# Optimization experiments

Measured on AMD Instinct MI355X. Metric: run time of the kernel, lower is better.

The kernel has to match this reference:

```python
import jax, jax.numpy as jnp
from jax import lax
import numpy as np

DN = ('NHWC', 'HWIO', 'NHWC')


def extract_patches(x, k, stride):
    # tf.image.extract_patches with sizes [1,k,k,1], strides [1,s,s,1], SAME padding.
    # Output depth ordering matches TF: (ki, kj, channel).
    B, H, W, C = x.shape
    oh = -(-H // stride)
    ow = -(-W // stride)
    ph = max((oh - 1) * stride + k - H, 0)
    pw = max((ow - 1) * stride + k - W, 0)
    xp = jnp.pad(x, ((0, 0), (ph // 2, ph - ph // 2), (pw // 2, pw - pw // 2), (0, 0)))
    cols = [xp[:, i:i + stride * (oh - 1) + 1:stride, j:j + stride * (ow - 1) + 1:stride, :]
            for i in range(k) for j in range(k)]
    return jnp.stack(cols, axis=3).reshape(B, oh, ow, k * k * C)


def contextual_attention(x, mask_s, rate=2, fuse_k=3, softmax_scale=10.0):
    B, H, W, C = x.shape
    k = rate * 2 - 1  # 3
    # raw (full-resolution) patches used as deconv filters: [B,k,k,C,L]
    raw = extract_patches(x, k, rate)
    h, w = raw.shape[1], raw.shape[2]
    L = h * w
    raw_f = raw.reshape(B, L, k, k, C).transpose(0, 2, 3, 4, 1)
    # downsample src/ref by rate (extract_patches with size 1 == strided slice)
    src = x[:, ::rate, ::rate, :]  # [B,h,w,C]
    feats = extract_patches(src, k, 1).reshape(B, L, k, k, C).transpose(0, 2, 3, 4, 1)  # [B,k,k,C,L]
    # NOTE: source normalizes by sum of squares over axes (0,1,2) = (batch,kh,kw) -> [C,L], no sqrt
    denom = jnp.maximum(jnp.sum(feats * feats, axis=(0, 1, 2)), 1e-8)
    ref_feat = feats / denom
    # mask: maxpool 16/16 then 3/1, then invert
    m = lax.reduce_window(mask_s, -jnp.inf, lax.max, (1, 16, 16, 1), (1, 16, 16, 1), 'SAME')
    m = lax.reduce_window(m, -jnp.inf, lax.max, (1, 3, 3, 1), (1, 1, 1, 1), 'SAME')
    mm = 1.0 - m  # [B,h,w,1]
    # per-sample correlation: conv src_b with its own normalized patch bank
    corr = lambda s, f: lax.conv_general_dilated(s[None], f, (1, 1), 'SAME', dimension_numbers=DN)[0]
    y = jax.vmap(corr)(src, ref_feat)  # [B,h,w,L]
    # fuse: diagonal (identity) 3x3 convs over the (query, key) score plane, both orderings
    fuse_w = jnp.eye(fuse_k, dtype=x.dtype).reshape(fuse_k, fuse_k, 1, 1)
    yi = y.reshape(B, h * w, L, 1)
    yi = lax.conv_general_dilated(yi, fuse_w, (1, 1), 'SAME', dimension_numbers=DN)
    yi = yi.reshape(B, h, w, h, w).transpose(0, 2, 1, 4, 3).reshape(B, h * w, L, 1)
    yi = lax.conv_general_dilated(yi, fuse_w, (1, 1), 'SAME', dimension_numbers=DN)
    y = yi.reshape(B, w, h, w, h).transpose(0, 2, 1, 4, 3).reshape(B, h, w, L)
    # masked softmax over reference patches
    y = jax.nn.softmax(y * mm * softmax_scale, axis=-1) * mm
    # per-sample transposed conv (paste raw patches), matching tf.nn.conv2d_transpose SAME stride=rate
    pt = max((h - 1) * rate + k - H, 0)
    pl = max((w - 1) * rate + k - W, 0)
    pad_h = (k - 1 - pt // 2, k - 1 - (pt - pt // 2))
    pad_w = (k - 1 - pl // 2, k - 1 - (pl - pl // 2))

    def deconv(y_b, f_b):
        wg = jnp.flip(f_b, axis=(0, 1)).swapaxes(2, 3)  # [k,k,L,C]
        return lax.conv_general_dilated(y_b[None], wg, (1, 1), (pad_h, pad_w),
                                        lhs_dilation=(rate, rate), dimension_numbers=DN)[0]

    y_up = jax.vmap(deconv)(y, raw_f)  # [B,H,W,C]
    return y_up, y


def gated_conv(x, w, b, dw, pw, db):
    # gen_conv_gated_ds: Conv2D -> ELU gated by SeparableConv2D -> channel softmax
    x1 = jax.nn.elu(lax.conv_general_dilated(x, w, (1, 1), 'SAME', dimension_numbers=DN) + b)
    x2 = lax.conv_general_dilated(x, dw, (1, 1), 'SAME', feature_group_count=x.shape[-1],
                                  dimension_numbers=DN)
    x2 = lax.conv_general_dilated(x2, pw, (1, 1), 'SAME', dimension_numbers=DN) + db
    return x1 * jax.nn.softmax(x2, axis=-1)


def setup_inputs():
    key = jax.random.key(0)
    ks = jax.random.split(key, 8)
    B, H, W, C, dim = 8, 64, 64, 128, 128
    s = 0.05
    x = jax.random.normal(ks[0], (B, H, W, C), jnp.float32)
    mask_s = jnp.zeros((B, 16 * H // 2, 16 * W // 2, 1), jnp.float32)
    mask_s = mask_s.at[:, 128:384, 128:384, :].set(1.0)
    return {
        'x': x,
        'mask_s': mask_s,
        'w1': jax.random.normal(ks[1], (3, 3, C, dim), jnp.float32) * s,
        'b1': jnp.zeros((dim,), jnp.float32),
        'dw1': jax.random.normal(ks[2], (3, 3, 1, C), jnp.float32) * s,
        'pw1': jax.random.normal(ks[3], (1, 1, C, dim), jnp.float32) * s,
        'db1': jnp.zeros((dim,), jnp.float32),
        'w2': jax.random.normal(ks[4], (3, 3, dim + C, dim), jnp.float32) * s,
        'b2': jnp.zeros((dim,), jnp.float32),
        'dw2': jax.random.normal(ks[5], (3, 3, 1, dim + C), jnp.float32) * s,
        'pw2': jax.random.normal(ks[6], (1, 1, dim + C, dim), jnp.float32) * s,
        'db2': jnp.zeros((dim,), jnp.float32),
    }


def reference(x, mask_s, w1, b1, dw1, pw1, db1, w2, b2, dw2, pw2, db2):
    y_up, corres = contextual_attention(x, mask_s)
    a = gated_conv(y_up, w1, b1, dw1, pw1, db1)
    a = jnp.concatenate([a, x], axis=3)
    a = gated_conv(a, w2, b2, dw2, pw2, db2)
    return a, corres
```

## Files before the change

kernel.cpp:

```cpp
#include <hip/hip_runtime.h>
#include <hip/hip_bf16.h>


#define BOFF_SP      0
#define BOFF_INVD    4734976
#define BOFF_SP16    5259264
#define BOFF_BF16    7626752
#define BOFF_T       0
#define BOFF_BP16    0
#define BOFF_YP16    33554432
#define BOFF_YUP     50331648
#define BOFF_SM      0
#define BOFF_P316    16777216
#define BOFF_A1      25698304
#define BOFF_X16     42475520
#define BOFF_WT1     69238784
#define BOFF_WT2     69828608
#define BOFF_PW1     71008256
#define BOFF_PW2     71041024
#define BOFF_M0      71106560
#define BOFF_MM      71139328

typedef float f32x4 __attribute__((ext_vector_type(4)));
typedef _Float16 f16x8 __attribute__((ext_vector_type(8)));

__global__ __launch_bounds__(256) void k_mask_pool(const float* __restrict__ mask, float* __restrict__ m0) {
    int blk = blockIdx.x;
    int b = blk >> 10, pq = blk & 1023, p = pq >> 5, q = pq & 31;
    int t = threadIdx.x, dy = t >> 4, dx = t & 15;
    float v = mask[((size_t)(b * 512 + p * 16 + dy)) * 512 + q * 16 + dx];
#pragma unroll
    for (int o = 32; o; o >>= 1) v = fmaxf(v, __shfl_xor(v, o));
    __shared__ float s[4];
    if ((t & 63) == 0) s[t >> 6] = v;
    __syncthreads();
    if (t == 0) m0[blk] = fmaxf(fmaxf(s[0], s[1]), fmaxf(s[2], s[3]));
}

__global__ void k_mask_dilate(const float* __restrict__ m0, float* __restrict__ mm) {
    int idx = blockIdx.x * 256 + threadIdx.x;
    if (idx >= 8192) return;
    int b = idx >> 10, pq = idx & 1023, p = pq >> 5, q = pq & 31;
    float v = -1e30f;
    for (int di = -1; di <= 1; ++di)
        for (int dj = -1; dj <= 1; ++dj) {
            int pp = p + di, qq = q + dj;
            if (pp >= 0 && pp < 32 && qq >= 0 && qq < 32)
                v = fmaxf(v, m0[(b << 10) + pp * 32 + qq]);
        }
    mm[idx] = 1.0f - v;
}

__global__ void k_srcpad(const float* __restrict__ x, float* __restrict__ sp,
                         _Float16* __restrict__ sp16) {
    int idx = blockIdx.x * 256 + threadIdx.x;
    if (idx >= 8 * 34 * 34 * 128) return;
    int c = idx & 127;
    int r = idx >> 7;
    int xx = r % 34; r /= 34;
    int yy = r % 34; int b = r / 34;
    float v = 0.f;
    if (yy >= 1 && yy <= 32 && xx >= 1 && xx <= 32)
        v = x[(((size_t)(b * 64 + (yy - 1) * 2)) * 64 + (xx - 1) * 2) * 128 + c];
    sp[idx] = v;
    sp16[idx] = (_Float16)v;
}

__global__ void k_invd(const float* __restrict__ sp, float* __restrict__ invd) {
    int idx = blockIdx.x * 256 + threadIdx.x;
    if (idx >= 1024 * 128) return;
    int c = idx & 127, l = idx >> 7, lh = l >> 5, lw = l & 31;
    float s = 0.f;
    for (int b = 0; b < 8; ++b)
#pragma unroll
        for (int i = 0; i < 3; ++i)
#pragma unroll
            for (int j = 0; j < 3; ++j) {
                float v = sp[(((size_t)(b * 34 + lh + i)) * 34 + (lw + j)) * 128 + c];
                s += v * v;
            }
    invd[idx] = 1.0f / fmaxf(s, 1e-8f);
}

__global__ void k_corr_B16(const float* __restrict__ sp, const float* __restrict__ invd,
                           _Float16* __restrict__ bf) {
    int idx = blockIdx.x * 256 + threadIdx.x;
    if (idx >= 1179648) return;
    int c8 = idx & 15; int rest = idx >> 4;
    int ij = rest % 9; int rest2 = rest / 9;
    int l = rest2 & 1023, b = rest2 >> 10;
    int lh = l >> 5, lw = l & 31;
    int i = (ij >= 6) ? 2 : (ij >= 3 ? 1 : 0);
    int j = ij - 3 * i;
    int c0 = c8 * 8;
    const float* s = sp + (((size_t)(b * 34 + lh + i)) * 34 + (lw + j)) * 128 + c0;
    const float* dv = invd + l * 128 + c0;
    f16x8 h;
#pragma unroll
    for (int u = 0; u < 8; ++u) h[u] = (_Float16)(s[u] * dv[u]);
    size_t off = ((size_t)(b * 1024 + l)) * 1152 + ij * 128 + c0;
    *reinterpret_cast<f16x8*>(bf + off) = h;
}

__global__ void k_deconv_B16(const float* __restrict__ x, _Float16* __restrict__ bp) {
    int idx = blockIdx.x * 256 + threadIdx.x;
    if (idx >= 1179648) return;
    int l8 = idx & 127; int rest = idx >> 7;
    int c = rest & 127; int rest2 = rest >> 7;
    int ij = rest2 % 9; int b = rest2 / 9;
    int ip = (ij >= 6) ? 2 : (ij >= 3 ? 1 : 0);
    int jp = ij - 3 * ip;
    int l0 = l8 * 8;
    int lh = l0 >> 5, lw0 = l0 & 31;
    int rr = 2 * lh + ip;
    f16x8 h;
#pragma unroll
    for (int u = 0; u < 8; ++u) {
        int ss = 2 * (lw0 + u) + jp;
        float v = (rr < 64 && ss < 64) ? x[(((size_t)(b * 64 + rr)) * 64 + ss) * 128 + c] : 0.f;
        h[u] = (_Float16)v;
    }
    size_t off = (((size_t)(b * 9 + ij)) * 128 + c) * 1024 + l0;
    *reinterpret_cast<f16x8*>(bp + off) = h;
}

__global__ __launch_bounds__(256) void k_corr_mfma(const _Float16* __restrict__ sp16,
                                                   const _Float16* __restrict__ bf,
                                                   float* __restrict__ outy) {
    const int bid = blockIdx.x;
    const int xcd = bid & 7, slot = bid >> 3;
    const int tm = slot & 15, pg = slot >> 4;
    const int panel = pg * 8 + xcd;
    const int b = panel >> 3, tn = panel & 7;
    __shared__ _Float16 Aa[64][40];
    __shared__ _Float16 Ab[64][40];
    const int tid = threadIdx.x;
    const int w = tid >> 6, lane = tid & 63, m = lane & 15, g = lane >> 4;
    f32x4 acc[4][2];
#pragma unroll
    for (int mf = 0; mf < 4; ++mf)
#pragma unroll
        for (int nn = 0; nn < 2; ++nn) acc[mf][nn] = f32x4{0.f, 0.f, 0.f, 0.f};
    const int srow = tid >> 2, scc = (tid & 3) * 8;
    const int pq = tm * 64 + srow, p = pq >> 5, q = pq & 31;
    const int col0 = tn * 128 + w * 32 + m;
    const size_t boff0 = ((size_t)b * 1024 + col0) * 1152 + g * 8;
    const size_t boff1 = ((size_t)b * 1024 + col0 + 16) * 1152 + g * 8;

    auto aoff = [&](int kt) -> size_t {
        int ij = kt >> 7;
        int i = (ij >= 6) ? 2 : (ij >= 3 ? 1 : 0);
        int j = ij - 3 * i;
        int c0 = (kt & 127) + scc;
        return (((size_t)(b * 34 + p + i)) * 34 + (q + j)) * 128 + c0;
    };
    f16x8 aq_a = *reinterpret_cast<const f16x8*>(sp16 + aoff(0));
    f16x8 aq_b = *reinterpret_cast<const f16x8*>(sp16 + aoff(32));
    f16x8 aq2_a = *reinterpret_cast<const f16x8*>(sp16 + aoff(64));
    f16x8 aq2_b = *reinterpret_cast<const f16x8*>(sp16 + aoff(96));
    f16x8 b0q_a = *reinterpret_cast<const f16x8*>(bf + boff0);
    f16x8 b0q_b = *reinterpret_cast<const f16x8*>(bf + boff0 + 32);
    f16x8 b1q_a = *reinterpret_cast<const f16x8*>(bf + boff1);
    f16x8 b1q_b = *reinterpret_cast<const f16x8*>(bf + boff1 + 32);
    f16x8 b0q2_a = *reinterpret_cast<const f16x8*>(bf + boff0 + 64);
    f16x8 b0q2_b = *reinterpret_cast<const f16x8*>(bf + boff0 + 96);
    f16x8 b1q2_a = *reinterpret_cast<const f16x8*>(bf + boff1 + 64);
    f16x8 b1q2_b = *reinterpret_cast<const f16x8*>(bf + boff1 + 96);

    for (int kt = 0; kt < 1152; kt += 64) {
        __syncthreads();
        *reinterpret_cast<f16x8*>(&Aa[srow][scc]) = aq_a;
        *reinterpret_cast<f16x8*>(&Ab[srow][scc]) = aq_b;
        __syncthreads();
        const int kt2 = (kt + 128 < 1152) ? kt + 128 : kt;
        f16x8 cb0a = b0q_a, cb0b = b0q_b, cb1a = b1q_a, cb1b = b1q_b;
        aq_a = aq2_a; aq_b = aq2_b;
        aq2_a = *reinterpret_cast<const f16x8*>(sp16 + aoff(kt2));
        aq2_b = *reinterpret_cast<const f16x8*>(sp16 + aoff(kt2 + 32));
        b0q_a = b0q2_a; b0q_b = b0q2_b;
        b1q_a = b1q2_a; b1q_b = b1q2_b;
        b0q2_a = *reinterpret_cast<const f16x8*>(bf + boff0 + kt2);
        b0q2_b = *reinterpret_cast<const f16x8*>(bf + boff0 + kt2 + 32);
        b1q2_a = *reinterpret_cast<const f16x8*>(bf + boff1 + kt2);
        b1q2_b = *reinterpret_cast<const f16x8*>(bf + boff1 + kt2 + 32);

        f16x8 av;
#pragma unroll
        for (int mf = 0; mf < 4; ++mf) {
            av = *reinterpret_cast<const f16x8*>(&Aa[mf * 16 + m][g * 8]);
            acc[mf][0] = __builtin_amdgcn_mfma_f32_16x16x32_f16(av, cb0a, acc[mf][0], 0, 0, 0);
            acc[mf][1] = __builtin_amdgcn_mfma_f32_16x16x32_f16(av, cb1a, acc[mf][1], 0, 0, 0);
            av = *reinterpret_cast<const f16x8*>(&Ab[mf * 16 + m][g * 8]);
            acc[mf][0] = __builtin_amdgcn_mfma_f32_16x16x32_f16(av, cb0b, acc[mf][0], 0, 0, 0);
            acc[mf][1] = __builtin_amdgcn_mfma_f32_16x16x32_f16(av, cb1b, acc[mf][1], 0, 0, 0);
        }
    }
#pragma unroll
    for (int mf = 0; mf < 4; ++mf) {
        int row = tm * 64 + mf * 16 + g * 4;
#pragma unroll
        for (int nn = 0; nn < 2; ++nn) {
            int col = col0 + nn * 16;
#pragma unroll
            for (int r = 0; r < 4; ++r)
                outy[((size_t)b << 20) + (size_t)(row + r) * 1024 + col] = acc[mf][nn][r];
        }
    }
}

__global__ __launch_bounds__(256) void k_deconv_mfma(const _Float16* __restrict__ yp16,
                                                     const _Float16* __restrict__ bp,
                                                     float* __restrict__ yup) {
    const int bid = blockIdx.x;
    const int b = bid & 7;
    const int slot = bid >> 3;
    const int tn = slot % 9;
    const int tm = slot / 9;
    __shared__ _Float16 Aa[64][40];
    __shared__ _Float16 Ab[64][40];
    const int tid = threadIdx.x;
    const int w = tid >> 6, lane = tid & 63, m = lane & 15, g = lane >> 4;
    f32x4 acc[4][2];
#pragma unroll
    for (int mf = 0; mf < 4; ++mf)
#pragma unroll
        for (int nn = 0; nn < 2; ++nn) acc[mf][nn] = f32x4{0.f, 0.f, 0.f, 0.f};
    const int srow = tid >> 2, scc = (tid & 3) * 8;
    const int c0 = w * 32 + m;
    const _Float16* abase = yp16 + ((size_t)b << 20) + (size_t)(tm * 64 + srow) * 1024 + scc;
    const size_t boff0 = (((size_t)(b * 9 + tn)) * 128 + c0) * 1024 + g * 8;
    const size_t boff1 = (((size_t)(b * 9 + tn)) * 128 + c0 + 16) * 1024 + g * 8;

    f16x8 aq_a = *reinterpret_cast<const f16x8*>(abase);
    f16x8 aq_b = *reinterpret_cast<const f16x8*>(abase + 32);
    f16x8 aq2_a = *reinterpret_cast<const f16x8*>(abase + 64);
    f16x8 aq2_b = *reinterpret_cast<const f16x8*>(abase + 96);
    f16x8 b0q_a = *reinterpret_cast<const f16x8*>(bp + boff0);
    f16x8 b0q_b = *reinterpret_cast<const f16x8*>(bp + boff0 + 32);
    f16x8 b1q_a = *reinterpret_cast<const f16x8*>(bp + boff1);
    f16x8 b1q_b = *reinterpret_cast<const f16x8*>(bp + boff1 + 32);
    f16x8 b0q2_a = *reinterpret_cast<const f16x8*>(bp + boff0 + 64);
    f16x8 b0q2_b = *reinterpret_cast<const f16x8*>(bp + boff0 + 96);
    f16x8 b1q2_a = *reinterpret_cast<const f16x8*>(bp + boff1 + 64);
    f16x8 b1q2_b = *reinterpret_cast<const f16x8*>(bp + boff1 + 96);

    for (int kt = 0; kt < 1024; kt += 64) {
        __syncthreads();
        *reinterpret_cast<f16x8*>(&Aa[srow][scc]) = aq_a;
        *reinterpret_cast<f16x8*>(&Ab[srow][scc]) = aq_b;
        __syncthreads();
        const int kt2 = (kt + 128 < 1024) ? kt + 128 : kt;
        f16x8 cb0a = b0q_a, cb0b = b0q_b, cb1a = b1q_a, cb1b = b1q_b;
        aq_a = aq2_a; aq_b = aq2_b;
        aq2_a = *reinterpret_cast<const f16x8*>(abase + kt2);
        aq2_b = *reinterpret_cast<const f16x8*>(abase + kt2 + 32);
        b0q_a = b0q2_a; b0q_b = b0q2_b;
        b1q_a = b1q2_a; b1q_b = b1q2_b;
        b0q2_a = *reinterpret_cast<const f16x8*>(bp + boff0 + kt2);
        b0q2_b = *reinterpret_cast<const f16x8*>(bp + boff0 + kt2 + 32);
        b1q2_a = *reinterpret_cast<const f16x8*>(bp + boff1 + kt2);
        b1q2_b = *reinterpret_cast<const f16x8*>(bp + boff1 + kt2 + 32);

        f16x8 av;
#pragma unroll
        for (int mf = 0; mf < 4; ++mf) {
            av = *reinterpret_cast<const f16x8*>(&Aa[mf * 16 + m][g * 8]);
            acc[mf][0] = __builtin_amdgcn_mfma_f32_16x16x32_f16(av, cb0a, acc[mf][0], 0, 0, 0);
            acc[mf][1] = __builtin_amdgcn_mfma_f32_16x16x32_f16(av, cb1a, acc[mf][1], 0, 0, 0);
            av = *reinterpret_cast<const f16x8*>(&Ab[mf * 16 + m][g * 8]);
            acc[mf][0] = __builtin_amdgcn_mfma_f32_16x16x32_f16(av, cb0b, acc[mf][0], 0, 0, 0);
            acc[mf][1] = __builtin_amdgcn_mfma_f32_16x16x32_f16(av, cb1b, acc[mf][1], 0, 0, 0);
        }
    }
    const int ip = (tn >= 6) ? 2 : (tn >= 3 ? 1 : 0);
    const int jp = tn - 3 * ip;
#pragma unroll
    for (int mf = 0; mf < 4; ++mf) {
        int uvb = tm * 64 + mf * 16 + g * 4;
#pragma unroll
        for (int nn = 0; nn < 2; ++nn) {
            int c = c0 + nn * 16;
#pragma unroll
            for (int r = 0; r < 4; ++r) {
                int uv = uvb + r;
                int uu = uv >> 5, vv = uv & 31;
                int P = 2 * uu + ip, Q = 2 * vv + jp;
                if (P < 64 && Q < 64)
                    atomicAdd(&yup[(((size_t)(b * 64 + P)) * 64 + Q) * 128 + c], acc[mf][nn][r]);
            }
        }
    }
}

__global__ void k_fuse12(const float* __restrict__ y, float* __restrict__ out) {
    size_t idx = (size_t)blockIdx.x * 256 + threadIdx.x;
    if (idx >= (size_t)8 * 1024 * 1024) return;
    int t = (int)(idx & 1023);
    int s = (int)((idx >> 10) & 1023);
    int b = (int)(idx >> 20);
    int m0 = ((s & 31) << 5) + (s >> 5);
    int n0 = ((t & 31) << 5) + (t >> 5);
    const float* base = y + ((size_t)b << 20);
    float v = 0.f;
#pragma unroll
    for (int d = -1; d <= 1; ++d) {
        int mm_ = m0 + d, nn_ = n0 + d;
        if (mm_ >= 0 && mm_ < 1024 && nn_ >= 0 && nn_ < 1024) {
            int a = ((mm_ & 31) << 5) + (mm_ >> 5);
            int c = ((nn_ & 31) << 5) + (nn_ >> 5);
            float zv = base[(size_t)a * 1024 + c];
            if (a > 0 && c > 0) zv += base[(size_t)(a - 1) * 1024 + (c - 1)];
            if (a < 1023 && c < 1023) zv += base[(size_t)(a + 1) * 1024 + (c + 1)];
            v += zv;
        }
    }
    out[idx] = v;
}

__global__ __launch_bounds__(256) void k_softmax1024(const float* __restrict__ yv,
                                                     const float* __restrict__ mm,
                                                     float* __restrict__ outc,
                                                     _Float16* __restrict__ yp16) {
    int row = blockIdx.x;
    const float* base = yv + (size_t)row * 1024;
    float mmv = mm[row];
    int t = threadIdx.x;
    float vals[4];
    float mx = -1e30f;
#pragma unroll
    for (int i = 0; i < 4; ++i) {
        vals[i] = base[t + i * 256] * mmv * 10.0f;
        mx = fmaxf(mx, vals[i]);
    }
#pragma unroll
    for (int o = 32; o; o >>= 1) mx = fmaxf(mx, __shfl_xor(mx, o));
    __shared__ float red[8];
    if ((t & 63) == 0) red[t >> 6] = mx;
    __syncthreads();
    mx = fmaxf(fmaxf(red[0], red[1]), fmaxf(red[2], red[3]));
    float s = 0.f;
#pragma unroll
    for (int i = 0; i < 4; ++i) {
        vals[i] = expf(vals[i] - mx);
        s += vals[i];
    }
#pragma unroll
    for (int o = 32; o; o >>= 1) s += __shfl_xor(s, o);
    if ((t & 63) == 0) red[4 + (t >> 6)] = s;
    __syncthreads();
    s = red[4] + red[5] + red[6] + red[7];
    float inv = mmv / s;
#pragma unroll
    for (int i = 0; i < 4; ++i) {
        float pv = vals[i] * inv;
        outc[(size_t)row * 1024 + t + i * 256] = pv;
        yp16[(size_t)row * 1024 + t + i * 256] = (_Float16)pv;
    }
}

__global__ __launch_bounds__(256) void k_pad16(const float* __restrict__ in,
                                               _Float16* __restrict__ o) {
    int idx = blockIdx.x * 256 + threadIdx.x;
    int c8 = idx & 15;
    int r = idx >> 4;
    int pc = r % 66; r /= 66;
    int pr = r % 66; int b = r / 66;
    f16x8 h;
    if (pr >= 1 && pr <= 64 && pc >= 1 && pc <= 64) {
        const float* s = in + (((size_t)(b * 64 + pr - 1)) * 64 + (pc - 1)) * 128 + c8 * 8;
        float4 v0 = *reinterpret_cast<const float4*>(s);
        float4 v1 = *reinterpret_cast<const float4*>(s + 4);
        h[0] = (_Float16)v0.x; h[1] = (_Float16)v0.y; h[2] = (_Float16)v0.z; h[3] = (_Float16)v0.w;
        h[4] = (_Float16)v1.x; h[5] = (_Float16)v1.y; h[6] = (_Float16)v1.z; h[7] = (_Float16)v1.w;
    } else {
#pragma unroll
        for (int u = 0; u < 8; ++u) h[u] = (_Float16)0.f;
    }
    *reinterpret_cast<f16x8*>(o + (size_t)idx * 8) = h;
}

__global__ void k_wt16(const float* __restrict__ w, _Float16* __restrict__ o, int CI) {
    int idx = blockIdx.x * 256 + threadIdx.x;
    if (idx >= 9 * CI * 128) return;
    int ci = idx % CI; int rest = idx / CI;
    int co = rest & 127; int ij = rest >> 7;
    o[idx] = (_Float16)w[((size_t)ij * CI + ci) * 128 + co];
}

__global__ void k_pw16(const float* __restrict__ pw, _Float16* __restrict__ out, int CI) {
    int idx = blockIdx.x * 256 + threadIdx.x;
    if (idx >= CI * 128) return;
    int co = idx & 127, ci = idx >> 7;
    out[(size_t)co * CI + ci] = (_Float16)pw[idx];
}

template <int CI>
__global__ __launch_bounds__(256) void k_dwpw_mfma(const _Float16* __restrict__ in0,
                                                   const _Float16* __restrict__ in1,
                                                   const float* __restrict__ dwW,
                                                   const _Float16* __restrict__ pwt,
                                                   const float* __restrict__ db,
                                                   float* __restrict__ smout) {
    const int bid = blockIdx.x;
    const int swz = (bid & 7) * 128 + (bid >> 3);
    const int b = swz >> 7;
    const int rem = swz & 127;
    const int P = rem >> 1, half = rem & 1;
    const int Q0 = half * 32;
    const int t = threadIdx.x;
    const int w = t >> 6, lane = t & 63, m = lane & 15, g = lane >> 4;
    __shared__ _Float16 Adw[32 * CI];
    __shared__ float red[2][4][32];
    char* ab = (char*)Adw;
    const int px = t & 31;
    const int grp = t >> 5;
    const int cb = grp * (CI / 8);
    float dwacc[CI / 8];
#pragma unroll
    for (int u = 0; u < CI / 8; ++u) dwacc[u] = 0.f;
#pragma unroll
    for (int i = 0; i < 3; ++i) {
#pragma unroll
        for (int j = 0; j < 3; ++j) {
            const int ij = i * 3 + j;
#pragma unroll
            for (int c8 = 0; c8 < CI / 64; ++c8) {
                const int c = cb + c8 * 8;
                const _Float16* ph = (CI == 256 && c >= 128) ? in1 : in0;
                const int cc = (CI == 256 && c >= 128) ? (c - 128) : c;
                size_t off = (((size_t)b * 66 + P + i) * 66 + Q0 + px + j) * 128 + cc;
                f16x8 vh = *reinterpret_cast<const f16x8*>(ph + off);
#pragma unroll
                for (int u = 0; u < 8; ++u)
                    dwacc[c8 * 8 + u] = fmaf((float)vh[u], dwW[ij * CI + c + u], dwacc[c8 * 8 + u]);
            }
        }
    }
#pragma unroll
    for (int c8 = 0; c8 < CI / 64; ++c8) {
        f16x8 hv;
#pragma unroll
        for (int u = 0; u < 8; ++u) hv[u] = (_Float16)dwacc[c8 * 8 + u];
        int byte = px * (CI * 2) + (cb + c8 * 8) * 2;
        int sz = byte ^ ((px & 7) << 4);
        *reinterpret_cast<f16x8*>(ab + sz) = hv;
    }
    __syncthreads();
    f32x4 acc[2][2];
#pragma unroll
    for (int mt = 0; mt < 2; ++mt)
#pragma unroll
        for (int nn = 0; nn < 2; ++nn) acc[mt][nn] = f32x4{0.f, 0.f, 0.f, 0.f};
    const int co0 = w * 32 + m;
#pragma unroll
    for (int kc = 0; kc < CI / 32; ++kc) {
        f16x8 av[2];
#pragma unroll
        for (int mt = 0; mt < 2; ++mt) {
            int prow = mt * 16 + m;
            int byte = prow * (CI * 2) + (kc * 32 + g * 8) * 2;
            int sz = byte ^ ((prow & 7) << 4);
            av[mt] = *reinterpret_cast<const f16x8*>(ab + sz);
        }
#pragma unroll
        for (int nn = 0; nn < 2; ++nn) {
            f16x8 bv = *reinterpret_cast<const f16x8*>(pwt + (size_t)(co0 + nn * 16) * CI + kc * 32 + g * 8);
#pragma unroll
            for (int mt = 0; mt < 2; ++mt)
                acc[mt][nn] = __builtin_amdgcn_mfma_f32_16x16x32_f16(av[mt], bv, acc[mt][nn], 0, 0, 0);
        }
    }
    float db0 = db[co0], db1 = db[co0 + 16];
    float mx[2][4];
#pragma unroll
    for (int mt = 0; mt < 2; ++mt)
#pragma unroll
        for (int r = 0; r < 4; ++r) {
            acc[mt][0][r] += db0;
            acc[mt][1][r] += db1;
            float v = fmaxf(acc[mt][0][r], acc[mt][1][r]);
#pragma unroll
            for (int o = 1; o <= 8; o <<= 1) v = fmaxf(v, __shfl_xor(v, o));
            mx[mt][r] = v;
        }
    if (m == 0) {
#pragma unroll
        for (int mt = 0; mt < 2; ++mt)
#pragma unroll
            for (int r = 0; r < 4; ++r) red[0][w][mt * 16 + g * 4 + r] = mx[mt][r];
    }
    __syncthreads();
    float sume[2][4];
#pragma unroll
    for (int mt = 0; mt < 2; ++mt)
#pragma unroll
        for (int r = 0; r < 4; ++r) {
            int p = mt * 16 + g * 4 + r;
            float M = fmaxf(fmaxf(red[0][0][p], red[0][1][p]), fmaxf(red[0][2][p], red[0][3][p]));
            acc[mt][0][r] = expf(acc[mt][0][r] - M);
            acc[mt][1][r] = expf(acc[mt][1][r] - M);
            float s = acc[mt][0][r] + acc[mt][1][r];
#pragma unroll
            for (int o = 1; o <= 8; o <<= 1) s += __shfl_xor(s, o);
            sume[mt][r] = s;
        }
    if (m == 0) {
#pragma unroll
        for (int mt = 0; mt < 2; ++mt)
#pragma unroll
            for (int r = 0; r < 4; ++r) red[1][w][mt * 16 + g * 4 + r] = sume[mt][r];
    }
    __syncthreads();
#pragma unroll
    for (int mt = 0; mt < 2; ++mt)
#pragma unroll
        for (int r = 0; r < 4; ++r) {
            int p = mt * 16 + g * 4 + r;
            float S = red[1][0][p] + red[1][1][p] + red[1][2][p] + red[1][3][p];
            float inv = 1.0f / S;
            size_t pix = ((size_t)b * 64 + P) * 64 + Q0 + p;
            smout[pix * 128 + co0] = acc[mt][0][r] * inv;
            smout[pix * 128 + co0 + 16] = acc[mt][1][r] * inv;
        }
}

template <int CI>
__global__ __launch_bounds__(256, 4) void k_conv_lds(const _Float16* __restrict__ in0,
                                                     const _Float16* __restrict__ in1,
                                                     const _Float16* __restrict__ wt,
                                                     const float* __restrict__ bias,
                                                     const float* __restrict__ sm,
                                                     float* __restrict__ out) {
    const int bid = blockIdx.x;
    const int idx = (bid & 7) * 128 + (bid >> 3);
    const int row = idx >> 1, cohalf = idx & 1;
    const int b = row >> 6, P = row & 63;
    const int tid = threadIdx.x;
    const int w = tid >> 6, lane = tid & 63;
    const int m = lane & 15, g = lane >> 4;
    __shared__ _Float16 S[66 * 128];
    char* sb = (char*)S;
    f32x4 acc[4];
#pragma unroll
    for (int mt = 0; mt < 4; ++mt) acc[mt] = f32x4{0.f, 0.f, 0.f, 0.f};
    const int cow = cohalf * 64 + w * 16 + m;

#pragma unroll
    for (int half = 0; half < CI / 128; ++half) {
        const _Float16* ih = (half == 0) ? in0 : in1;
        const size_t rbase0 = ((size_t)b * 66 + P) * 66 * 128;
#pragma unroll
        for (int i = 0; i < 3; ++i) {
            __syncthreads();
            const size_t rsrc = rbase0 + (size_t)i * 66 * 128;
#pragma unroll
            for (int e0 = 0; e0 < 1056; e0 += 256) {
                int e = e0 + tid;
                if (e < 1056) {
                    int px = e >> 4, c8 = e & 15;
                    int lin = px * 256 + c8 * 16;
                    int sz = lin ^ ((px & 7) << 4);
                    size_t so = rsrc + (size_t)px * 128 + c8 * 8;
                    *reinterpret_cast<f16x8*>(sb + sz) = *reinterpret_cast<const f16x8*>(ih + so);
                }
            }
            __syncthreads();
#pragma unroll
            for (int j = 0; j < 3; ++j) {
                const int ij = i * 3 + j;
                const _Float16* wp = wt + ((size_t)ij * 128 + cow) * CI + half * 128 + g * 8;
#pragma unroll
                for (int ci0 = 0; ci0 < 128; ci0 += 32) {
                    f16x8 bv = *reinterpret_cast<const f16x8*>(wp + ci0);
                    f16x8 av[4];
#pragma unroll
                    for (int mt = 0; mt < 4; ++mt) {
                        int px = mt * 16 + m + j;
                        int lin = px * 256 + ci0 * 2 + g * 16;
                        int sz = lin ^ ((px & 7) << 4);
                        av[mt] = *reinterpret_cast<const f16x8*>(sb + sz);
                    }
#pragma unroll
                    for (int mt = 0; mt < 4; ++mt)
                        acc[mt] = __builtin_amdgcn_mfma_f32_16x16x32_f16(av[mt], bv, acc[mt], 0, 0, 0);
                }
            }
        }
    }
    const float bb = bias[cow];
#pragma unroll
    for (int mt = 0; mt < 4; ++mt) {
#pragma unroll
        for (int r = 0; r < 4; ++r) {
            int Q = mt * 16 + g * 4 + r;
            size_t pix = ((size_t)b * 64 + P) * 64 + Q;
            float z = acc[mt][r] + bb;
            z = z > 0.f ? z : expm1f(z);
            out[pix * 128 + cow] = z * sm[pix * 128 + cow];
        }
    }
}

extern "C" void kernel_launch(void* const* d_in, const int* in_sizes, int n_in,
                              void* d_out, int out_size, void* d_ws, size_t ws_size,
                              hipStream_t stream) {
    const float* x    = (const float*)d_in[0];
    const float* mask = (const float*)d_in[1];
    const float* w1   = (const float*)d_in[2];
    const float* b1   = (const float*)d_in[3];
    const float* dw1  = (const float*)d_in[4];
    const float* pw1  = (const float*)d_in[5];
    const float* db1  = (const float*)d_in[6];
    const float* w2   = (const float*)d_in[7];
    const float* b2   = (const float*)d_in[8];
    const float* dw2  = (const float*)d_in[9];
    const float* pw2  = (const float*)d_in[10];
    const float* db2  = (const float*)d_in[11];

    float* out_a = (float*)d_out;
    float* out_c = out_a + 4194304;

    char* wsb = (char*)d_ws;
    float* sp      = (float*)(wsb + BOFF_SP);
    float* invd    = (float*)(wsb + BOFF_INVD);
    _Float16* sp16 = (_Float16*)(wsb + BOFF_SP16);
    _Float16* bf16b = (_Float16*)(wsb + BOFF_BF16);
    float* Tbuf    = (float*)(wsb + BOFF_T);
    _Float16* bp16 = (_Float16*)(wsb + BOFF_BP16);
    _Float16* yp16 = (_Float16*)(wsb + BOFF_YP16);
    float* yup     = (float*)(wsb + BOFF_YUP);
    float* smb     = (float*)(wsb + BOFF_SM);
    _Float16* p316 = (_Float16*)(wsb + BOFF_P316);
    float* a1      = (float*)(wsb + BOFF_A1);
    _Float16* x16  = (_Float16*)(wsb + BOFF_X16);
    _Float16* wt1  = (_Float16*)(wsb + BOFF_WT1);
    _Float16* wt2  = (_Float16*)(wsb + BOFF_WT2);
    _Float16* pw1t = (_Float16*)(wsb + BOFF_PW1);
    _Float16* pw2t = (_Float16*)(wsb + BOFF_PW2);
    float* m0      = (float*)(wsb + BOFF_M0);
    float* mmb     = (float*)(wsb + BOFF_MM);

    k_mask_pool<<<8192, 256, 0, stream>>>(mask, m0);
    k_mask_dilate<<<32, 256, 0, stream>>>(m0, mmb);
    k_srcpad<<<4624, 256, 0, stream>>>(x, sp, sp16);
    k_invd<<<512, 256, 0, stream>>>(sp, invd);
    k_wt16<<<576, 256, 0, stream>>>(w1, wt1, 128);
    k_wt16<<<1152, 256, 0, stream>>>(w2, wt2, 256);
    k_pw16<<<64, 256, 0, stream>>>(pw1, pw1t, 128);
    k_pw16<<<128, 256, 0, stream>>>(pw2, pw2t, 256);
    k_corr_B16<<<4608, 256, 0, stream>>>(sp, invd, bf16b);
    k_corr_mfma<<<1024, 256, 0, stream>>>(sp16, bf16b, out_c);
    k_fuse12<<<32768, 256, 0, stream>>>(out_c, Tbuf);
    k_softmax1024<<<8192, 256, 0, stream>>>(Tbuf, mmb, out_c, yp16);
    k_deconv_B16<<<4608, 256, 0, stream>>>(x, bp16);
    hipMemsetAsync(yup, 0, (size_t)4194304 * sizeof(float), stream);
    k_deconv_mfma<<<1152, 256, 0, stream>>>(yp16, bp16, yup);
    k_pad16<<<2178, 256, 0, stream>>>(yup, p316);
    k_pad16<<<2178, 256, 0, stream>>>(x, x16);
    k_dwpw_mfma<128><<<1024, 256, 0, stream>>>(p316, nullptr, dw1, pw1t, db1, smb);
    k_conv_lds<128><<<1024, 256, 0, stream>>>(p316, nullptr, wt1, b1, smb, a1);
    k_pad16<<<2178, 256, 0, stream>>>(a1, p316);
    k_dwpw_mfma<256><<<1024, 256, 0, stream>>>(p316, x16, dw2, pw2t, db2, smb);
    k_conv_lds<256><<<1024, 256, 0, stream>>>(p316, x16, wt2, b2, smb, out_a);
}
```

Before: 388.4 us.

## Fuse diagonal score fusion into softmax and emit padded fp16 from first conv

Merges the fuse12 kernel into the softmax kernel, so each row computes its diagonal-summed scores on the fly. This drops the full-size fp32 intermediate write and read. The first gated conv now writes fp16 straight into a zeroed, padded buffer, which removes the fp32 a1 buffer and a pad kernel. The workspace layout is reshuffled to fit the new buffers, and an extra memset is added to zero the pad border. Uncoalesced gather reads now run inside the softmax blocks, which may lower its efficiency.

```diff
diff --git a/kernel.cpp b/kernel.cpp
--- a/kernel.cpp
+++ b/kernel.cpp
@@ -2,17 +2,17 @@
 #include <hip/hip_bf16.h>
 
 
-#define BOFF_SP      0
-#define BOFF_INVD    4734976
-#define BOFF_SP16    5259264
-#define BOFF_BF16    7626752
 #define BOFF_T       0
+#define BOFF_SP      33554432
+#define BOFF_INVD    38289408
+#define BOFF_SP16    38813696
+#define BOFF_BF16    41181184
+#define BOFF_YP16    33554432
 #define BOFF_BP16    0
-#define BOFF_YP16    33554432
 #define BOFF_YUP     50331648
 #define BOFF_SM      0
 #define BOFF_P316    16777216
-#define BOFF_A1      25698304
+#define BOFF_P316B   25698304
 #define BOFF_X16     42475520
 #define BOFF_WT1     69238784
 #define BOFF_WT2     69828608
@@ -292,69 +292,61 @@
     }
 }
 
-__global__ void k_fuse12(const float* __restrict__ y, float* __restrict__ out) {
-    size_t idx = (size_t)blockIdx.x * 256 + threadIdx.x;
-    if (idx >= (size_t)8 * 1024 * 1024) return;
-    int t = (int)(idx & 1023);
-    int s = (int)((idx >> 10) & 1023);
-    int b = (int)(idx >> 20);
-    int m0 = ((s & 31) << 5) + (s >> 5);
-    int n0 = ((t & 31) << 5) + (t >> 5);
+__global__ __launch_bounds__(256) void k_fsm(const float* __restrict__ y,
+                                             const float* __restrict__ mm,
+                                             float* __restrict__ outc,
+                                             _Float16* __restrict__ yp16) {
+    int row = blockIdx.x;
+    int b = row >> 10, s = row & 1023;
     const float* base = y + ((size_t)b << 20);
-    float v = 0.f;
-#pragma unroll
-    for (int d = -1; d <= 1; ++d) {
-        int mm_ = m0 + d, nn_ = n0 + d;
-        if (mm_ >= 0 && mm_ < 1024 && nn_ >= 0 && nn_ < 1024) {
-            int a = ((mm_ & 31) << 5) + (mm_ >> 5);
-            int c = ((nn_ & 31) << 5) + (nn_ >> 5);
-            float zv = base[(size_t)a * 1024 + c];
-            if (a > 0 && c > 0) zv += base[(size_t)(a - 1) * 1024 + (c - 1)];
-            if (a < 1023 && c < 1023) zv += base[(size_t)(a + 1) * 1024 + (c + 1)];
-            v += zv;
-        }
-    }
-    out[idx] = v;
-}
-
-__global__ __launch_bounds__(256) void k_softmax1024(const float* __restrict__ yv,
-                                                     const float* __restrict__ mm,
-                                                     float* __restrict__ outc,
-                                                     _Float16* __restrict__ yp16) {
-    int row = blockIdx.x;
-    const float* base = yv + (size_t)row * 1024;
     float mmv = mm[row];
-    int t = threadIdx.x;
+    int t0 = threadIdx.x;
+    const int m0 = ((s & 31) << 5) + (s >> 5);
     float vals[4];
     float mx = -1e30f;
 #pragma unroll
     for (int i = 0; i < 4; ++i) {
-        vals[i] = base[t + i * 256] * mmv * 10.0f;
+        int t = t0 + i * 256;
+        int n0 = ((t & 31) << 5) + (t >> 5);
+        float v = 0.f;
+#pragma unroll
+        for (int d = -1; d <= 1; ++d) {
+            int mm_ = m0 + d, nn_ = n0 + d;
+            if (mm_ >= 0 && mm_ < 1024 && nn_ >= 0 && nn_ < 1024) {
+                int a = ((mm_ & 31) << 5) + (mm_ >> 5);
+                int c = ((nn_ & 31) << 5) + (nn_ >> 5);
+                float zv = base[(size_t)a * 1024 + c];
+                if (a > 0 && c > 0) zv += base[(size_t)(a - 1) * 1024 + (c - 1)];
+                if (a < 1023 && c < 1023) zv += base[(size_t)(a + 1) * 1024 + (c + 1)];
+                v += zv;
+            }
+        }
+        vals[i] = v * mmv * 10.0f;
         mx = fmaxf(mx, vals[i]);
     }
 #pragma unroll
     for (int o = 32; o; o >>= 1) mx = fmaxf(mx, __shfl_xor(mx, o));
     __shared__ float red[8];
-    if ((t & 63) == 0) red[t >> 6] = mx;
+    if ((t0 & 63) == 0) red[t0 >> 6] = mx;
     __syncthreads();
     mx = fmaxf(fmaxf(red[0], red[1]), fmaxf(red[2], red[3]));
-    float s = 0.f;
+    float ssum = 0.f;
 #pragma unroll
     for (int i = 0; i < 4; ++i) {
         vals[i] = expf(vals[i] - mx);
-        s += vals[i];
-    }
-#pragma unroll
-    for (int o = 32; o; o >>= 1) s += __shfl_xor(s, o);
-    if ((t & 63) == 0) red[4 + (t >> 6)] = s;
+        ssum += vals[i];
+    }
+#pragma unroll
+    for (int o = 32; o; o >>= 1) ssum += __shfl_xor(ssum, o);
+    if ((t0 & 63) == 0) red[4 + (t0 >> 6)] = ssum;
     __syncthreads();
-    s = red[4] + red[5] + red[6] + red[7];
-    float inv = mmv / s;
+    ssum = red[4] + red[5] + red[6] + red[7];
+    float inv = mmv / ssum;
 #pragma unroll
     for (int i = 0; i < 4; ++i) {
         float pv = vals[i] * inv;
-        outc[(size_t)row * 1024 + t + i * 256] = pv;
-        yp16[(size_t)row * 1024 + t + i * 256] = (_Float16)pv;
+        outc[(size_t)row * 1024 + t0 + i * 256] = pv;
+        yp16[(size_t)row * 1024 + t0 + i * 256] = (_Float16)pv;
     }
 }
 
@@ -524,13 +516,14 @@
         }
 }
 
-template <int CI>
+template <int CI, int W16>
 __global__ __launch_bounds__(256, 4) void k_conv_lds(const _Float16* __restrict__ in0,
                                                      const _Float16* __restrict__ in1,
                                                      const _Float16* __restrict__ wt,
                                                      const float* __restrict__ bias,
                                                      const float* __restrict__ sm,
-                                                     float* __restrict__ out) {
+                                                     float* __restrict__ out,
+                                                     _Float16* __restrict__ out16) {
     const int bid = blockIdx.x;
     const int idx = (bid & 7) * 128 + (bid >> 3);
     const int row = idx >> 1, cohalf = idx & 1;
@@ -596,7 +589,12 @@
             size_t pix = ((size_t)b * 64 + P) * 64 + Q;
             float z = acc[mt][r] + bb;
             z = z > 0.f ? z : expm1f(z);
-            out[pix * 128 + cow] = z * sm[pix * 128 + cow];
+            float res = z * sm[pix * 128 + cow];
+            if (W16) {
+                out16[(((size_t)b * 66 + P + 1) * 66 + Q + 1) * 128 + cow] = (_Float16)res;
+            } else {
+                out[pix * 128 + cow] = res;
+            }
         }
     }
 }
@@ -621,17 +619,17 @@
     float* out_c = out_a + 4194304;
 
     char* wsb = (char*)d_ws;
+    float* Tbuf    = (float*)(wsb + BOFF_T);
     float* sp      = (float*)(wsb + BOFF_SP);
     float* invd    = (float*)(wsb + BOFF_INVD);
     _Float16* sp16 = (_Float16*)(wsb + BOFF_SP16);
     _Float16* bf16b = (_Float16*)(wsb + BOFF_BF16);
-    float* Tbuf    = (float*)(wsb + BOFF_T);
+    _Float16* yp16 = (_Float16*)(wsb + BOFF_YP16);
     _Float16* bp16 = (_Float16*)(wsb + BOFF_BP16);
-    _Float16* yp16 = (_Float16*)(wsb + BOFF_YP16);
     float* yup     = (float*)(wsb + BOFF_YUP);
     float* smb     = (float*)(wsb + BOFF_SM);
     _Float16* p316 = (_Float16*)(wsb + BOFF_P316);
-    float* a1      = (float*)(wsb + BOFF_A1);
+    _Float16* p316b = (_Float16*)(wsb + BOFF_P316B);
     _Float16* x16  = (_Float16*)(wsb + BOFF_X16);
     _Float16* wt1  = (_Float16*)(wsb + BOFF_WT1);
     _Float16* wt2  = (_Float16*)(wsb + BOFF_WT2);
@@ -649,17 +647,17 @@
     k_pw16<<<64, 256, 0, stream>>>(pw1, pw1t, 128);
     k_pw16<<<128, 256, 0, stream>>>(pw2, pw2t, 256);
     k_corr_B16<<<4608, 256, 0, stream>>>(sp, invd, bf16b);
-    k_corr_mfma<<<1024, 256, 0, stream>>>(sp16, bf16b, out_c);
-    k_fuse12<<<32768, 256, 0, stream>>>(out_c, Tbuf);
-    k_softmax1024<<<8192, 256, 0, stream>>>(Tbuf, mmb, out_c, yp16);
+    k_corr_mfma<<<1024, 256, 0, stream>>>(sp16, bf16b, Tbuf);
+    k_fsm<<<8192, 256, 0, stream>>>(Tbuf, mmb, out_c, yp16);
     k_deconv_B16<<<4608, 256, 0, stream>>>(x, bp16);
     hipMemsetAsync(yup, 0, (size_t)4194304 * sizeof(float), stream);
     k_deconv_mfma<<<1152, 256, 0, stream>>>(yp16, bp16, yup);
     k_pad16<<<2178, 256, 0, stream>>>(yup, p316);
     k_pad16<<<2178, 256, 0, stream>>>(x, x16);
+    hipMemsetAsync(p316b, 0, (size_t)8 * 66 * 66 * 128 * sizeof(_Float16), stream);
     k_dwpw_mfma<128><<<1024, 256, 0, stream>>>(p316, nullptr, dw1, pw1t, db1, smb);
-    k_conv_lds<128><<<1024, 256, 0, stream>>>(p316, nullptr, wt1, b1, smb, a1);
-    k_pad16<<<2178, 256, 0, stream>>>(a1, p316);
-    k_dwpw_mfma<256><<<1024, 256, 0, stream>>>(p316, x16, dw2, pw2t, db2, smb);
-    k_conv_lds<256><<<1024, 256, 0, stream>>>(p316, x16, wt2, b2, smb, out_a);
-}
+    k_conv_lds<128, 1><<<1024, 256, 0, stream>>>(p316, nullptr, wt1, b1, smb,
+                                                 nullptr, p316b);
+    k_dwpw_mfma<256><<<1024, 256, 0, stream>>>(p316b, x16, dw2, pw2t, db2, smb);
+    k_conv_lds<256, 0><<<1024, 256, 0, stream>>>(p316b, x16, wt2, b2, smb, out_a, nullptr);
+}
```

Result: faster. 371.1 us (median of 3 runs) (-4.4%).
